# Kernel tuning notes

Measured on AMD Instinct MI355X. Metric: run time of the kernel, lower is better.

Reference implementation:

```python
import jax, jax.numpy as jnp
import numpy as np

D = 128; H = 4; HD = 32; K = 4; OUT = 2; COND = 6; FF = 256

def _ln(x, g, b):
    m = x.mean(-1, keepdims=True)
    v = ((x - m) ** 2).mean(-1, keepdims=True)
    return g * (x - m) * jax.lax.rsqrt(v + 1e-5) + b

def setup_inputs() -> dict:
    key = jax.random.key(0)
    ks = jax.random.split(key, 40)
    B, S = 4096, 128
    def w(k, shape, scale=0.05):
        return (jax.random.normal(k, shape, dtype=jnp.float32) * scale)
    inp = {
        'x': jax.random.normal(ks[0], (B, OUT, S), dtype=jnp.float32),
        'timesteps': jax.random.randint(ks[1], (B,), 0, 1000, dtype=jnp.int32),
        'conditions': jax.random.normal(ks[2], (B, S, COND), dtype=jnp.float32),
        # time embedding MLP: Linear(128->256), SiLU, Linear(256->128)
        't_w1': w(ks[3], (D, 2 * D)), 't_b1': jnp.zeros((2 * D,), jnp.float32),
        't_w2': w(ks[4], (2 * D, D)), 't_b2': jnp.zeros((D,), jnp.float32),
        # condition MLP: Linear(6->64), SiLU, Linear(64->128), SiLU
        'c_w1': w(ks[5], (COND, D // 2)), 'c_b1': jnp.zeros((D // 2,), jnp.float32),
        'c_w2': w(ks[6], (D // 2, D)), 'c_b2': jnp.zeros((D,), jnp.float32),
        # 2 transformer encoder layers (post-norm, relu FFN, dropout=0 eval)
        'attn_wqkv': w(ks[7], (2, D, 3 * D)), 'attn_bqkv': jnp.zeros((2, 3 * D), jnp.float32),
        'attn_wo': w(ks[8], (2, D, D)), 'attn_bo': jnp.zeros((2, D), jnp.float32),
        'ln1_g': jnp.ones((2, D), jnp.float32), 'ln1_b': jnp.zeros((2, D), jnp.float32),
        'ff_w1': w(ks[9], (2, D, FF)), 'ff_b1': jnp.zeros((2, FF), jnp.float32),
        'ff_w2': w(ks[10], (2, FF, D)), 'ff_b2': jnp.zeros((2, D), jnp.float32),
        'ln2_g': jnp.ones((2, D), jnp.float32), 'ln2_b': jnp.zeros((2, D), jnp.float32),
        # mixture weights net: Linear(256->128), SiLU, Linear(128->4), Softmax
        'mw_w1': w(ks[11], (2 * D, D)), 'mw_b1': jnp.zeros((D,), jnp.float32),
        'mw_w2': w(ks[12], (D, K)), 'mw_b2': jnp.zeros((K,), jnp.float32),
        # K student networks: Linear(2+256->128), Tanh, Linear(128->2)
        's_w1': w(ks[13], (K, OUT + 2 * D, D)), 's_b1': jnp.zeros((K, D), jnp.float32),
        's_w2': w(ks[14], (K, D, OUT)), 's_b2': jnp.zeros((K, OUT), jnp.float32),
    }
    return inp

def reference(x, timesteps, conditions, t_w1, t_b1, t_w2, t_b2, c_w1, c_b1, c_w2, c_b2,
              attn_wqkv, attn_bqkv, attn_wo, attn_bo, ln1_g, ln1_b, ff_w1, ff_b1,
              ff_w2, ff_b2, ln2_g, ln2_b, mw_w1, mw_b1, mw_w2, mw_b2,
              s_w1, s_b1, s_w2, s_b2):
    B, _, S = x.shape
    # sinusoidal time embedding
    half = D // 2
    freqs = jnp.exp(-jnp.log(jnp.float32(10000.0)) * jnp.arange(half, dtype=jnp.float32) / half)
    args = timesteps.astype(jnp.float32)[:, None] * freqs[None, :]
    te = jnp.concatenate([jnp.cos(args), jnp.sin(args)], axis=-1)            # [B, D]
    time_emb = jax.nn.silu(te @ t_w1 + t_b1) @ t_w2 + t_b2                   # [B, D]
    # condition embedding MLP
    h = jax.nn.silu(conditions @ c_w1 + c_b1)
    h = jax.nn.silu(h @ c_w2 + c_b2)                                          # [B, S, D]
    # 2-layer transformer encoder (post-norm)
    for l in range(2):
        qkv = h @ attn_wqkv[l] + attn_bqkv[l]                                 # [B, S, 3D]
        q, k, v = jnp.split(qkv, 3, axis=-1)
        q = q.reshape(B, S, H, HD); k = k.reshape(B, S, H, HD); v = v.reshape(B, S, H, HD)
        sc = jnp.einsum('bqhd,bkhd->bhqk', q, k) / jnp.sqrt(jnp.float32(HD))
        a = jax.nn.softmax(sc, axis=-1)
        o = jnp.einsum('bhqk,bkhd->bqhd', a, v).reshape(B, S, D)
        o = o @ attn_wo[l] + attn_bo[l]
        h = _ln(h + o, ln1_g[l], ln1_b[l])
        f = jax.nn.relu(h @ ff_w1[l] + ff_b1[l]) @ ff_w2[l] + ff_b2[l]
        h = _ln(h + f, ln2_g[l], ln2_b[l])
    cond_emb = h.mean(axis=1)                                                 # [B, D]
    combined = jnp.concatenate([time_emb, cond_emb], axis=-1)                 # [B, 2D]
    mw = jax.nn.softmax(jax.nn.silu(combined @ mw_w1 + mw_b1) @ mw_w2 + mw_b2, axis=-1)  # [B, K]
    # students over all seq positions (vectorized over original seq loop)
    xt = jnp.transpose(x, (0, 2, 1))                                          # [B, S, OUT]
    emb_bs = jnp.broadcast_to(combined[:, None, :], (B, S, 2 * D))
    inp = jnp.concatenate([xt, emb_bs], axis=-1)                              # [B, S, OUT+2D]
    hk = jnp.tanh(jnp.einsum('bsi,kio->bsko', inp, s_w1) + s_b1)              # [B, S, K, D]
    ok = jnp.einsum('bsko,koj->bskj', hk, s_w2) + s_b2                        # [B, S, K, OUT]
    out = jnp.einsum('bskj,bk->bsj', ok, mw)                                  # [B, S, OUT]
    return jnp.transpose(out, (0, 2, 1))                                      # [B, OUT, S]
```

## Files before the change

kernel.cpp:

```cpp
#include <hip/hip_runtime.h>

typedef _Float16 hf;
typedef _Float16 hf4 __attribute__((ext_vector_type(4)));
typedef _Float16 hf8 __attribute__((ext_vector_type(8)));
typedef float f4 __attribute__((ext_vector_type(4)));

#define NTH 512
#define ACT_OFF 0
#define P_OFF   32768
#define SC_OFF  40960
#define SMEM_BYTES 73728

#define WSH_QKV 0
#define WSH_WO  98304
#define WSH_FW1 131072
#define WSH_FW2 196608
#define WSH_CW2 262144
#define WSH_TOTAL 270336
#define CEMB_BYTE_OFF 540672

__device__ __forceinline__ float dsilu(float x){ return x / (1.f + __expf(-x)); }
__device__ __forceinline__ float dtanh(float x){
  float xc = fminf(fmaxf(x, -10.f), 10.f);
  float e = __expf(2.f * xc);
  return (e - 1.f) / (e + 1.f);
}

__global__ void prep_pack(const float* __restrict__ wqkv, const float* __restrict__ wo,
                          const float* __restrict__ fw1, const float* __restrict__ fw2,
                          const float* __restrict__ cw2, hf* __restrict__ ws){
  int idx = blockIdx.x * 256 + threadIdx.x;
  if (idx >= WSH_TOTAL) return;
  float v;
  if (idx < WSH_WO){
    int u = idx; int lh = u / 12288; int l = lh >> 2, h = lh & 3;
    int r = u % 12288; int tl = r >> 9; int lane = (r >> 3) & 63; int j = r & 7;
    int q = lane >> 4, c = lane & 15;
    int tn = tl >> 2, tk = tl & 3;
    int k = tk*32 + q*8 + j, nloc = tn*16 + c;
    int gcol = (nloc >> 5)*128 + h*32 + (nloc & 31);
    v = wqkv[l*49152 + k*384 + gcol];
  } else if (idx < WSH_FW1){
    int u = idx - WSH_WO; int l = u >> 14; int r = u & 16383;
    int tl = r >> 9; int lane = (r >> 3) & 63; int j = r & 7;
    int q = lane >> 4, c = lane & 15;
    int tn = tl >> 2, tk = tl & 3;
    v = wo[l*16384 + (tk*32 + q*8 + j)*128 + tn*16 + c];
  } else if (idx < WSH_FW2){
    int u = idx - WSH_FW1; int lch = u >> 14; int l = lch >> 1, ch = lch & 1; int r = u & 16383;
    int tl = r >> 9; int lane = (r >> 3) & 63; int j = r & 7;
    int q = lane >> 4, c = lane & 15;
    int tn = tl >> 2, tk = tl & 3;
    v = fw1[l*32768 + (tk*32 + q*8 + j)*256 + ch*128 + tn*16 + c];
  } else if (idx < WSH_CW2){
    int u = idx - WSH_FW2; int lch = u >> 14; int l = lch >> 1, ch = lch & 1; int r = u & 16383;
    int tl = r >> 9; int lane = (r >> 3) & 63; int j = r & 7;
    int q = lane >> 4, c = lane & 15;
    int tn = tl >> 2, tk = tl & 3;
    v = fw2[l*32768 + (ch*128 + tk*32 + q*8 + j)*128 + tn*16 + c];
  } else {
    int u = idx - WSH_CW2;
    int tl = u >> 9; int lane = (u >> 3) & 63; int j = u & 7;
    int q = lane >> 4, c = lane & 15;
    int tn = tl >> 1, tk = tl & 1;
    v = cw2[(tk*32 + q*8 + j)*128 + tn*16 + c];
  }
  ws[idx] = (hf)v;
}

template<int KT>
__device__ __forceinline__ void gemmN(f4 (&acc)[8], const hf* __restrict__ Ag, const hf* Bh,
                                      int nt, int lane){
#pragma unroll
  for (int tk = 0; tk < KT; ++tk){
    hf8 a = *(const hf8*)(Ag + ((nt*KT + tk) << 9) + lane*8);
#pragma unroll
    for (int ts = 0; ts < 8; ++ts){
      hf8 b = *(const hf8*)(Bh + ((ts*KT + tk) << 9) + lane*8);
      acc[ts] = __builtin_amdgcn_mfma_f32_16x16x32_f16(a, b, acc[ts], 0, 0, 0);
    }
  }
}

__device__ __forceinline__ void store_packed_b64(hf* dst, int KtilesOut, int ts, int ft,
                                                 f4 v, int q, int c){
  int tk = ft >> 1;
  int qp = ((ft & 1) << 1) + (q >> 1);
  int j0 = (q & 1) << 2;
  hf4 h; h[0] = (hf)v[0]; h[1] = (hf)v[1]; h[2] = (hf)v[2]; h[3] = (hf)v[3];
  *(hf4*)(dst + ((ts*KtilesOut + tk) << 9) + ((qp*16 + c) << 3) + j0) = h;
}

__device__ __forceinline__ void ln_pass(hf* A, const hf* Dh, const float* __restrict__ g,
                                        const float* __restrict__ bb, int t){
  int s = t >> 2, p = t & 3;
  float xr[4][8];
  int offs[4];
  float sum = 0.f, sq = 0.f;
#pragma unroll
  for (int tk = 0; tk < 4; ++tk){
    int off = (((s >> 4) * 4 + tk) << 9) + ((p * 16 + (s & 15)) << 3);
    offs[tk] = off;
    hf8 va = *(const hf8*)(A + off);
    hf8 vd = *(const hf8*)(Dh + off);
#pragma unroll
    for (int j = 0; j < 8; ++j){
      float x = (float)va[j] + (float)vd[j];
      xr[tk][j] = x; sum += x; sq += x * x;
    }
  }
  sum += __shfl_xor(sum, 1); sq += __shfl_xor(sq, 1);
  sum += __shfl_xor(sum, 2); sq += __shfl_xor(sq, 2);
  float mean = sum * (1.f/128.f);
  float rstd = rsqrtf(sq * (1.f/128.f) - mean*mean + 1e-5f);
#pragma unroll
  for (int tk = 0; tk < 4; ++tk){
    int f0 = tk*32 + p*8;
    f4 g0 = *(const f4*)(g + f0); f4 g1 = *(const f4*)(g + f0 + 4);
    f4 b0 = *(const f4*)(bb + f0); f4 b1 = *(const f4*)(bb + f0 + 4);
    hf8 y;
#pragma unroll
    for (int j = 0; j < 4; ++j){
      y[j]     = (hf)((xr[tk][j]     - mean) * rstd * g0[j] + b0[j]);
      y[j + 4] = (hf)((xr[tk][j + 4] - mean) * rstd * g1[j] + b1[j]);
    }
    *(hf8*)(A + offs[tk]) = y;
  }
}

__global__ __launch_bounds__(NTH, 4) void fused_fp(
    const float* __restrict__ cond,
    const float* __restrict__ c_w1, const float* __restrict__ c_b1, const float* __restrict__ c_b2,
    const float* __restrict__ bqkv_g, const float* __restrict__ bo_g,
    const float* __restrict__ ln1g_g, const float* __restrict__ ln1b_g,
    const float* __restrict__ fb1_g, const float* __restrict__ fb2_g,
    const float* __restrict__ ln2g_g, const float* __restrict__ ln2b_g,
    const hf* __restrict__ wsp, float* __restrict__ cemb)
{
  extern __shared__ char smem[];
  hf* ACTh = (hf*)(smem + ACT_OFF);
  hf* Ph   = (hf*)(smem + P_OFF);
  hf* SCh  = (hf*)(smem + SC_OFF);
  float* SCf = (float*)(smem + SC_OFF);
  hf* Qh  = SCh;
  hf* Kh  = (hf*)(smem + SC_OFF + 8192);
  hf* VTh = (hf*)(smem + SC_OFF + 16384);
  float* cst  = SCf + 4096;
  float* cw1s = SCf + 4096 + 768;

  const int b = blockIdx.x;
  const int t = threadIdx.x;
  const int w = t >> 6, lane = t & 63, q = lane >> 4, c = lane & 15;
  const int sp = w & 3, np = w >> 2;

  for (int idx = t; idx < 768; idx += NTH) cst[idx] = cond[b * 768 + idx];
  if (t < 384) cw1s[t] = c_w1[t];
  if (t < 64)  cw1s[384 + t] = c_b1[t];
  __syncthreads();

  for (int idx = t; idx < 8192; idx += NTH){
    int s = idx >> 6, jf = idx & 63;
    float a = cw1s[384 + jf];
#pragma unroll
    for (int cc = 0; cc < 6; ++cc) a += cst[s * 6 + cc] * cw1s[cc * 64 + jf];
    SCh[(((s >> 4)*2 + (jf >> 5)) << 9) + ((((jf & 31) >> 3)*16 + (s & 15)) << 3) + (jf & 7)] = (hf)dsilu(a);
  }
  __syncthreads();

  {
    f4 acc[8];
#pragma unroll
    for (int i = 0; i < 8; ++i){ f4 z = {0.f,0.f,0.f,0.f}; acc[i] = z; }
    gemmN<2>(acc, wsp + WSH_CW2, SCh, w, lane);
    f4 cb = *(const f4*)(c_b2 + w*16 + q*4);
#pragma unroll
    for (int ts = 0; ts < 8; ++ts){
      f4 v = acc[ts];
#pragma unroll
      for (int r = 0; r < 4; ++r) v[r] = dsilu(v[r] + cb[r]);
      store_packed_b64(ACTh, 4, ts, w, v, q, c);
    }
  }

  for (int l = 0; l < 2; ++l){
    f4 oacc[8];
#pragma unroll
    for (int i = 0; i < 8; ++i){ f4 z = {0.f,0.f,0.f,0.f}; oacc[i] = z; }

    for (int h = 0; h < 4; ++h){
      __syncthreads();
      {
        const hf* Aq = wsp + WSH_QKV + (l*4 + h)*12288;
        f4 acc[2][3];
#pragma unroll
        for (int i = 0; i < 2; ++i)
#pragma unroll
          for (int j = 0; j < 3; ++j){ f4 z = {0.f,0.f,0.f,0.f}; acc[i][j] = z; }
#pragma unroll
        for (int tk = 0; tk < 4; ++tk){
          hf8 b0 = *(const hf8*)(ACTh + (((2*sp  )*4 + tk) << 9) + lane*8);
          hf8 b1 = *(const hf8*)(ACTh + (((2*sp+1)*4 + tk) << 9) + lane*8);
#pragma unroll
          for (int jn = 0; jn < 3; ++jn){
            hf8 a = *(const hf8*)(Aq + (((np*3 + jn)*4 + tk) << 9) + lane*8);
            acc[0][jn] = __builtin_amdgcn_mfma_f32_16x16x32_f16(a, b0, acc[0][jn], 0, 0, 0);
            acc[1][jn] = __builtin_amdgcn_mfma_f32_16x16x32_f16(a, b1, acc[1][jn], 0, 0, 0);
          }
        }
#pragma unroll
        for (int si = 0; si < 2; ++si)
#pragma unroll
          for (int jn = 0; jn < 3; ++jn){
            int ft = np*3 + jn, ts = 2*sp + si;
            int sel = ft >> 1;
            f4 v = acc[si][jn];
            f4 bq = *(const f4*)(bqkv_g + l*384 + sel*128 + h*32 + (ft & 1)*16 + q*4);
#pragma unroll
            for (int r = 0; r < 4; ++r) v[r] += bq[r];
            if (sel == 0){
#pragma unroll
              for (int r = 0; r < 4; ++r) v[r] *= 0.17677669529663687f;
              store_packed_b64(Qh, 1, ts, ft, v, q, c);
            } else if (sel == 1){
              store_packed_b64(Kh, 1, ts, ft - 2, v, q, c);
            } else {
              int td = ft - 4;
              int qp = ((ts & 1) << 1) + (c >> 3);
              hf* pb = VTh + ((td*4 + (ts >> 1)) << 9) + (c & 7);
#pragma unroll
              for (int r = 0; r < 4; ++r) pb[(qp*16 + q*4 + r) << 3] = (hf)v[r];
            }
          }
      }
      __syncthreads();
      {
        hf8 qf = *(const hf8*)(Qh + (w << 9) + lane*8);
        f4 sc[8];
#pragma unroll
        for (int kst = 0; kst < 8; ++kst){
          hf8 kv = *(const hf8*)(Kh + (kst << 9) + lane*8);
          f4 z = {0.f,0.f,0.f,0.f};
          sc[kst] = __builtin_amdgcn_mfma_f32_16x16x32_f16(kv, qf, z, 0, 0, 0);
        }
        float m = -1e30f;
#pragma unroll
        for (int kst = 0; kst < 8; ++kst)
#pragma unroll
          for (int r = 0; r < 4; ++r) m = fmaxf(m, sc[kst][r]);
        m = fmaxf(m, __shfl_xor(m, 16));
        m = fmaxf(m, __shfl_xor(m, 32));
        float ls = 0.f;
#pragma unroll
        for (int kst = 0; kst < 8; ++kst)
#pragma unroll
          for (int r = 0; r < 4; ++r){
            float e = __expf(sc[kst][r] - m);
            sc[kst][r] = e; ls += e;
          }
        ls += __shfl_xor(ls, 16);
        ls += __shfl_xor(ls, 32);
        float rl = 1.f / ls;
        hf* Pw = Ph + (w << 9);
#pragma unroll
        for (int ks = 0; ks < 4; ++ks){
#pragma unroll
          for (int h2 = 0; h2 < 2; ++h2){
            int kst = 2*ks + h2;
            int qp = h2*2 + (q >> 1);
            int j0 = (q & 1) << 2;
            hf4 pv;
#pragma unroll
            for (int r = 0; r < 4; ++r) pv[r] = (hf)(sc[kst][r] * rl);
            *(hf4*)(Pw + qp*128 + c*8 + j0) = pv;
          }
          hf8 bp = *(const hf8*)(Pw + lane*8);
          hf8 a0 = *(const hf8*)(VTh + ((     ks) << 9) + lane*8);
          hf8 a1 = *(const hf8*)(VTh + ((4 +  ks) << 9) + lane*8);
          oacc[2*h]     = __builtin_amdgcn_mfma_f32_16x16x32_f16(a0, bp, oacc[2*h],     0, 0, 0);
          oacc[2*h + 1] = __builtin_amdgcn_mfma_f32_16x16x32_f16(a1, bp, oacc[2*h + 1], 0, 0, 0);
        }
      }
    }

    __syncthreads();
#pragma unroll
    for (int ft = 0; ft < 8; ++ft) store_packed_b64(SCh, 4, w, ft, oacc[ft], q, c);
    __syncthreads();

    {
      f4 acc[8];
#pragma unroll
      for (int i = 0; i < 8; ++i){ f4 z = {0.f,0.f,0.f,0.f}; acc[i] = z; }
      gemmN<4>(acc, wsp + WSH_WO + l*16384, SCh, w, lane);
      __syncthreads();
      f4 bo = *(const f4*)(bo_g + l*128 + w*16 + q*4);
#pragma unroll
      for (int ts = 0; ts < 8; ++ts){
        f4 v = acc[ts];
#pragma unroll
        for (int r = 0; r < 4; ++r) v[r] += bo[r];
        store_packed_b64(SCh, 4, ts, w, v, q, c);
      }
    }
    __syncthreads();
    ln_pass(ACTh, SCh, ln1g_g + l*128, ln1b_g + l*128, t);
    __syncthreads();

    {
      f4 facc[8];
#pragma unroll
      for (int i = 0; i < 8; ++i){ f4 z = {0.f,0.f,0.f,0.f}; facc[i] = z; }
      for (int ch = 0; ch < 2; ++ch){
        f4 acc[8];
#pragma unroll
        for (int i = 0; i < 8; ++i){ f4 z = {0.f,0.f,0.f,0.f}; acc[i] = z; }
        gemmN<4>(acc, wsp + WSH_FW1 + (l*2 + ch)*16384, ACTh, w, lane);
        f4 fb = *(const f4*)(fb1_g + l*256 + ch*128 + w*16 + q*4);
#pragma unroll
        for (int ts = 0; ts < 8; ++ts){
          f4 v = acc[ts];
#pragma unroll
          for (int r = 0; r < 4; ++r) v[r] = fmaxf(v[r] + fb[r], 0.f);
          store_packed_b64(SCh, 4, ts, w, v, q, c);
        }
        __syncthreads();
        gemmN<4>(facc, wsp + WSH_FW2 + (l*2 + ch)*16384, SCh, w, lane);
        __syncthreads();
      }
      f4 fb2 = *(const f4*)(fb2_g + l*128 + w*16 + q*4);
#pragma unroll
      for (int ts = 0; ts < 8; ++ts){
        f4 v = facc[ts];
#pragma unroll
        for (int r = 0; r < 4; ++r) v[r] += fb2[r];
        store_packed_b64(SCh, 4, ts, w, v, q, c);
      }
    }
    __syncthreads();
    ln_pass(ACTh, SCh, ln2g_g + l*128, ln2b_g + l*128, t);
    __syncthreads();
  }

  {
    int o = t & 15;
    float fs[8];
#pragma unroll
    for (int j = 0; j < 8; ++j) fs[j] = 0.f;
#pragma unroll
    for (int u = 0; u < 4; ++u){
      int s = (t >> 4)*4 + u;
      hf8 v = *(const hf8*)(ACTh + (((s >> 4)*4 + (o >> 2)) << 9) + (((o & 3)*16 + (s & 15)) << 3));
#pragma unroll
      for (int j = 0; j < 8; ++j) fs[j] += (float)v[j];
    }
#pragma unroll
    for (int j = 0; j < 8; ++j){
      fs[j] += __shfl_xor(fs[j], 16);
      fs[j] += __shfl_xor(fs[j], 32);
    }
    if (lane < 16){
      f4 v0, v1;
#pragma unroll
      for (int j = 0; j < 4; ++j){ v0[j] = fs[j]; v1[j] = fs[j+4]; }
      *(f4*)(SCf + w*128 + o*8)     = v0;
      *(f4*)(SCf + w*128 + o*8 + 4) = v1;
    }
  }
  __syncthreads();
  if (t < 128){
    float a = 0.f;
#pragma unroll
    for (int wv = 0; wv < 8; ++wv) a += SCf[wv*128 + t];
    cemb[b*128 + t] = a * (1.f/128.f);
  }
}

__global__ __launch_bounds__(256, 4) void tail_k(
    const float* __restrict__ x, const int* __restrict__ tstep, const float* __restrict__ cemb,
    const float* __restrict__ t_w1, const float* __restrict__ t_b1,
    const float* __restrict__ t_w2, const float* __restrict__ t_b2,
    const float* __restrict__ mw_w1, const float* __restrict__ mw_b1,
    const float* __restrict__ mw_w2, const float* __restrict__ mw_b2,
    const float* __restrict__ s_w1, const float* __restrict__ s_b1,
    const float* __restrict__ s_w2, const float* __restrict__ s_b2,
    float* __restrict__ out)
{
  __shared__ float sw01[1024], sw2[1024];
  __shared__ float te[128], th[256], comb[256], mwh[128], mwls[8], cvec[512], okp[1024];
  const int t = threadIdx.x;

  for (int i = t; i < 1024; i += 256){
    int row = i >> 9, k = (i >> 7) & 3, j = i & 127;
    sw01[i] = s_w1[k*33024 + row*128 + j];
    sw2[i]  = s_w2[i];
  }
  __syncthreads();

  for (int bi = 0; bi < 8; ++bi){
    int b = blockIdx.x * 8 + bi;
    if (t < 128){
      int i = t & 63;
      float f = __expf(-logf(10000.f) * (float)i * (1.f/64.f));
      float a = (float)tstep[b] * f;
      te[t] = (t < 64) ? cosf(a) : sinf(a);
    }
    __syncthreads();
    {
      float a = t_b1[t];
      for (int i = 0; i < 128; ++i) a += te[i] * t_w1[i*256 + t];
      th[t] = dsilu(a);
    }
    __syncthreads();
    if (t < 128){
      float a = t_b2[t];
      for (int j = 0; j < 256; ++j) a += th[j] * t_w2[j*128 + t];
      comb[t] = a;
    } else {
      comb[t] = cemb[b*128 + t - 128];
    }
    __syncthreads();
    if (t < 128){
      float a = mw_b1[t];
      for (int i = 0; i < 256; ++i) a += comb[i] * mw_w1[i*128 + t];
      mwh[t] = dsilu(a);
    }
#pragma unroll
    for (int u = 0; u < 2; ++u){
      int o = t + u*256; int k = o >> 7, j = o & 127;
      float a = s_b1[k*128 + j];
      for (int i = 0; i < 256; ++i) a += comb[i] * s_w1[k*33024 + (2 + i)*128 + j];
      cvec[o] = a;
    }
    __syncthreads();
    if (t < 4){
      float a = mw_b2[t];
      for (int j = 0; j < 128; ++j) a += mwh[j] * mw_w2[j*4 + t];
      mwls[4 + t] = a;
    }
    __syncthreads();
    if (t == 0){
      float mx = fmaxf(fmaxf(mwls[4], mwls[5]), fmaxf(mwls[6], mwls[7]));
      float e0 = __expf(mwls[4] - mx), e1 = __expf(mwls[5] - mx);
      float e2 = __expf(mwls[6] - mx), e3 = __expf(mwls[7] - mx);
      float rs = 1.f / (e0 + e1 + e2 + e3);
      mwls[0] = e0*rs; mwls[1] = e1*rs; mwls[2] = e2*rs; mwls[3] = e3*rs;
    }
#pragma unroll
    for (int u = 0; u < 2; ++u){
      int o = t + u*256; int k = o >> 7, s = o & 127;
      float x0 = x[b*256 + s];
      float x1 = x[b*256 + 128 + s];
      float a0 = 0.f, a1 = 0.f;
      for (int j = 0; j < 128; ++j){
        float hk = dtanh(cvec[k*128 + j] + x0*sw01[k*128 + j] + x1*sw01[512 + k*128 + j]);
        a0 += hk * sw2[k*256 + 2*j];
        a1 += hk * sw2[k*256 + 2*j + 1];
      }
      okp[k*256 + s]       = a0 + s_b2[2*k];
      okp[k*256 + 128 + s] = a1 + s_b2[2*k + 1];
    }
    __syncthreads();
    {
      int row = t >> 7, s = t & 127;
      float a = 0.f;
#pragma unroll
      for (int k = 0; k < 4; ++k) a += mwls[k] * okp[k*256 + row*128 + s];
      out[b*256 + row*128 + s] = a;
    }
    __syncthreads();
  }
}

extern "C" void kernel_launch(void* const* d_in, const int* in_sizes, int n_in,
                              void* d_out, int out_size, void* d_ws, size_t ws_size,
                              hipStream_t stream){
  (void)n_in; (void)ws_size; (void)out_size;
  hipFuncSetAttribute((const void*)fused_fp, hipFuncAttributeMaxDynamicSharedMemorySize, SMEM_BYTES);
  int B = in_sizes[1];
  hf* wsp = (hf*)d_ws;
  float* cemb = (float*)((char*)d_ws + CEMB_BYTE_OFF);
  prep_pack<<<dim3((WSH_TOTAL + 255) / 256), dim3(256), 0, stream>>>(
      (const float*)d_in[11], (const float*)d_in[13], (const float*)d_in[17],
      (const float*)d_in[19], (const float*)d_in[9], wsp);
  fused_fp<<<dim3(B), dim3(NTH), SMEM_BYTES, stream>>>(
      (const float*)d_in[2],
      (const float*)d_in[7], (const float*)d_in[8], (const float*)d_in[10],
      (const float*)d_in[12], (const float*)d_in[14],
      (const float*)d_in[15], (const float*)d_in[16],
      (const float*)d_in[18], (const float*)d_in[20],
      (const float*)d_in[21], (const float*)d_in[22],
      wsp, cemb);
  tail_k<<<dim3(B / 8), dim3(256), 0, stream>>>(
      (const float*)d_in[0], (const int*)d_in[1], cemb,
      (const float*)d_in[3], (const float*)d_in[4], (const float*)d_in[5], (const float*)d_in[6],
      (const float*)d_in[23], (const float*)d_in[24], (const float*)d_in[25], (const float*)d_in[26],
      (const float*)d_in[27], (const float*)d_in[28], (const float*)d_in[29], (const float*)d_in[30],
      (float*)d_out);
}
```

Before: 1.201 ms.

## Fuse time-embedding, mixture and student tail into the per-sample transformer kernel

```diff
diff --git a/kernel.cpp b/kernel.cpp
--- a/kernel.cpp
+++ b/kernel.cpp
@@ -9,7 +9,8 @@
 #define ACT_OFF 0
 #define P_OFF   32768
 #define SC_OFF  40960
-#define SMEM_BYTES 73728
+#define COMB_OFF 73728
+#define SMEM_BYTES 74752
 
 #define WSH_QKV 0
 #define WSH_WO  98304
@@ -17,7 +18,6 @@
 #define WSH_FW2 196608
 #define WSH_CW2 262144
 #define WSH_TOTAL 270336
-#define CEMB_BYTE_OFF 540672
 
 __device__ __forceinline__ float dsilu(float x){ return x / (1.f + __expf(-x)); }
 __device__ __forceinline__ float dtanh(float x){
@@ -129,24 +129,39 @@
 }
 
 __global__ __launch_bounds__(NTH, 4) void fused_fp(
-    const float* __restrict__ cond,
+    const float* __restrict__ x, const int* __restrict__ tstep, const float* __restrict__ cond,
+    const float* __restrict__ t_w1, const float* __restrict__ t_b1,
+    const float* __restrict__ t_w2, const float* __restrict__ t_b2,
     const float* __restrict__ c_w1, const float* __restrict__ c_b1, const float* __restrict__ c_b2,
     const float* __restrict__ bqkv_g, const float* __restrict__ bo_g,
     const float* __restrict__ ln1g_g, const float* __restrict__ ln1b_g,
     const float* __restrict__ fb1_g, const float* __restrict__ fb2_g,
     const float* __restrict__ ln2g_g, const float* __restrict__ ln2b_g,
-    const hf* __restrict__ wsp, float* __restrict__ cemb)
+    const float* __restrict__ mw_w1, const float* __restrict__ mw_b1,
+    const float* __restrict__ mw_w2, const float* __restrict__ mw_b2,
+    const float* __restrict__ s_w1, const float* __restrict__ s_b1,
+    const float* __restrict__ s_w2, const float* __restrict__ s_b2,
+    const hf* __restrict__ wsp, float* __restrict__ out)
 {
   extern __shared__ char smem[];
   hf* ACTh = (hf*)(smem + ACT_OFF);
   hf* Ph   = (hf*)(smem + P_OFF);
   hf* SCh  = (hf*)(smem + SC_OFF);
   float* SCf = (float*)(smem + SC_OFF);
+  float* comb = (float*)(smem + COMB_OFF);
   hf* Qh  = SCh;
   hf* Kh  = (hf*)(smem + SC_OFF + 8192);
   hf* VTh = (hf*)(smem + SC_OFF + 16384);
   float* cst  = SCf + 4096;
-  float* cw1s = SCf + 4096 + 768;
+  float* cw1s = SCf + 4864;
+  float* te   = SCf + 5312;
+  float* th   = SCf + 5440;
+  float* sw01 = SCf;
+  float* sw2t = SCf + 1024;
+  float* cvec = SCf + 2048;
+  float* okp  = SCf + 2560;
+  float* mwh  = SCf + 3584;
+  float* mwls = SCf + 3712;
 
   const int b = blockIdx.x;
   const int t = threadIdx.x;
@@ -156,6 +171,12 @@
   for (int idx = t; idx < 768; idx += NTH) cst[idx] = cond[b * 768 + idx];
   if (t < 384) cw1s[t] = c_w1[t];
   if (t < 64)  cw1s[384 + t] = c_b1[t];
+  if (t < 128){
+    int i = t & 63;
+    float f = __expf(-logf(10000.f) * (float)i * (1.f/64.f));
+    float a = (float)tstep[b] * f;
+    te[t] = (t < 64) ? cosf(a) : sinf(a);
+  }
   __syncthreads();
 
   for (int idx = t; idx < 8192; idx += NTH){
@@ -165,6 +186,11 @@
     for (int cc = 0; cc < 6; ++cc) a += cst[s * 6 + cc] * cw1s[cc * 64 + jf];
     SCh[(((s >> 4)*2 + (jf >> 5)) << 9) + ((((jf & 31) >> 3)*16 + (s & 15)) << 3) + (jf & 7)] = (hf)dsilu(a);
   }
+  if (t < 256){
+    float a = t_b1[t];
+    for (int i = 0; i < 128; ++i) a += te[i] * t_w1[i*256 + t];
+    th[t] = dsilu(a);
+  }
   __syncthreads();
 
   {
@@ -180,6 +206,11 @@
       for (int r = 0; r < 4; ++r) v[r] = dsilu(v[r] + cb[r]);
       store_packed_b64(ACTh, 4, ts, w, v, q, c);
     }
+  }
+  if (t < 128){
+    float a = t_b2[t];
+    for (int j = 0; j < 256; ++j) a += th[j] * t_w2[j*128 + t];
+    comb[t] = a;
   }
 
   for (int l = 0; l < 2; ++l){
@@ -371,103 +402,57 @@
     float a = 0.f;
 #pragma unroll
     for (int wv = 0; wv < 8; ++wv) a += SCf[wv*128 + t];
-    cemb[b*128 + t] = a * (1.f/128.f);
-  }
-}
-
-__global__ __launch_bounds__(256, 4) void tail_k(
-    const float* __restrict__ x, const int* __restrict__ tstep, const float* __restrict__ cemb,
-    const float* __restrict__ t_w1, const float* __restrict__ t_b1,
-    const float* __restrict__ t_w2, const float* __restrict__ t_b2,
-    const float* __restrict__ mw_w1, const float* __restrict__ mw_b1,
-    const float* __restrict__ mw_w2, const float* __restrict__ mw_b2,
-    const float* __restrict__ s_w1, const float* __restrict__ s_b1,
-    const float* __restrict__ s_w2, const float* __restrict__ s_b2,
-    float* __restrict__ out)
-{
-  __shared__ float sw01[1024], sw2[1024];
-  __shared__ float te[128], th[256], comb[256], mwh[128], mwls[8], cvec[512], okp[1024];
-  const int t = threadIdx.x;
-
-  for (int i = t; i < 1024; i += 256){
+    comb[128 + t] = a * (1.f/128.f);
+  }
+  __syncthreads();
+
+  for (int i = t; i < 1024; i += NTH){
     int row = i >> 9, k = (i >> 7) & 3, j = i & 127;
     sw01[i] = s_w1[k*33024 + row*128 + j];
-    sw2[i]  = s_w2[i];
-  }
-  __syncthreads();
-
-  for (int bi = 0; bi < 8; ++bi){
-    int b = blockIdx.x * 8 + bi;
-    if (t < 128){
-      int i = t & 63;
-      float f = __expf(-logf(10000.f) * (float)i * (1.f/64.f));
-      float a = (float)tstep[b] * f;
-      te[t] = (t < 64) ? cosf(a) : sinf(a);
-    }
-    __syncthreads();
-    {
-      float a = t_b1[t];
-      for (int i = 0; i < 128; ++i) a += te[i] * t_w1[i*256 + t];
-      th[t] = dsilu(a);
-    }
-    __syncthreads();
-    if (t < 128){
-      float a = t_b2[t];
-      for (int j = 0; j < 256; ++j) a += th[j] * t_w2[j*128 + t];
-      comb[t] = a;
-    } else {
-      comb[t] = cemb[b*128 + t - 128];
-    }
-    __syncthreads();
-    if (t < 128){
-      float a = mw_b1[t];
-      for (int i = 0; i < 256; ++i) a += comb[i] * mw_w1[i*128 + t];
-      mwh[t] = dsilu(a);
-    }
-#pragma unroll
-    for (int u = 0; u < 2; ++u){
-      int o = t + u*256; int k = o >> 7, j = o & 127;
-      float a = s_b1[k*128 + j];
-      for (int i = 0; i < 256; ++i) a += comb[i] * s_w1[k*33024 + (2 + i)*128 + j];
-      cvec[o] = a;
-    }
-    __syncthreads();
-    if (t < 4){
-      float a = mw_b2[t];
-      for (int j = 0; j < 128; ++j) a += mwh[j] * mw_w2[j*4 + t];
-      mwls[4 + t] = a;
-    }
-    __syncthreads();
-    if (t == 0){
-      float mx = fmaxf(fmaxf(mwls[4], mwls[5]), fmaxf(mwls[6], mwls[7]));
-      float e0 = __expf(mwls[4] - mx), e1 = __expf(mwls[5] - mx);
-      float e2 = __expf(mwls[6] - mx), e3 = __expf(mwls[7] - mx);
-      float rs = 1.f / (e0 + e1 + e2 + e3);
-      mwls[0] = e0*rs; mwls[1] = e1*rs; mwls[2] = e2*rs; mwls[3] = e3*rs;
-    }
-#pragma unroll
-    for (int u = 0; u < 2; ++u){
-      int o = t + u*256; int k = o >> 7, s = o & 127;
-      float x0 = x[b*256 + s];
-      float x1 = x[b*256 + 128 + s];
-      float a0 = 0.f, a1 = 0.f;
-      for (int j = 0; j < 128; ++j){
-        float hk = dtanh(cvec[k*128 + j] + x0*sw01[k*128 + j] + x1*sw01[512 + k*128 + j]);
-        a0 += hk * sw2[k*256 + 2*j];
-        a1 += hk * sw2[k*256 + 2*j + 1];
-      }
-      okp[k*256 + s]       = a0 + s_b2[2*k];
-      okp[k*256 + 128 + s] = a1 + s_b2[2*k + 1];
-    }
-    __syncthreads();
-    {
-      int row = t >> 7, s = t & 127;
-      float a = 0.f;
-#pragma unroll
-      for (int k = 0; k < 4; ++k) a += mwls[k] * okp[k*256 + row*128 + s];
-      out[b*256 + row*128 + s] = a;
-    }
-    __syncthreads();
+    sw2t[i] = s_w2[i];
+  }
+  if (t < 128){
+    float a = mw_b1[t];
+    for (int i = 0; i < 256; ++i) a += comb[i] * mw_w1[i*128 + t];
+    mwh[t] = dsilu(a);
+  }
+  {
+    int k = t >> 7, j = t & 127;
+    float a = s_b1[k*128 + j];
+    for (int i = 0; i < 256; ++i) a += comb[i] * s_w1[k*33024 + (2 + i)*128 + j];
+    cvec[t] = a;
+  }
+  __syncthreads();
+
+  if (t < 4){
+    float a = mw_b2[t];
+    for (int j = 0; j < 128; ++j) a += mwh[j] * mw_w2[j*4 + t];
+    mwls[t] = a;
+  }
+  {
+    int k = t >> 7, s = t & 127;
+    float x0 = x[b*256 + s];
+    float x1 = x[b*256 + 128 + s];
+    float a0 = 0.f, a1 = 0.f;
+    for (int j = 0; j < 128; ++j){
+      float hk = dtanh(cvec[k*128 + j] + x0*sw01[k*128 + j] + x1*sw01[512 + k*128 + j]);
+      a0 += hk * sw2t[k*256 + 2*j];
+      a1 += hk * sw2t[k*256 + 2*j + 1];
+    }
+    okp[k*256 + s]       = a0 + s_b2[2*k];
+    okp[k*256 + 128 + s] = a1 + s_b2[2*k + 1];
+  }
+  __syncthreads();
+
+  if (t < 256){
+    int row = t >> 7, s = t & 127;
+    float l0 = mwls[0], l1 = mwls[1], l2 = mwls[2], l3 = mwls[3];
+    float mx = fmaxf(fmaxf(l0, l1), fmaxf(l2, l3));
+    float e0 = __expf(l0 - mx), e1 = __expf(l1 - mx), e2 = __expf(l2 - mx), e3 = __expf(l3 - mx);
+    float rs = 1.f / (e0 + e1 + e2 + e3);
+    float a = e0*okp[0*256 + row*128 + s] + e1*okp[1*256 + row*128 + s]
+            + e2*okp[2*256 + row*128 + s] + e3*okp[3*256 + row*128 + s];
+    out[b*256 + row*128 + s] = a * rs;
   }
 }
 
@@ -478,22 +463,18 @@
   hipFuncSetAttribute((const void*)fused_fp, hipFuncAttributeMaxDynamicSharedMemorySize, SMEM_BYTES);
   int B = in_sizes[1];
   hf* wsp = (hf*)d_ws;
-  float* cemb = (float*)((char*)d_ws + CEMB_BYTE_OFF);
   prep_pack<<<dim3((WSH_TOTAL + 255) / 256), dim3(256), 0, stream>>>(
       (const float*)d_in[11], (const float*)d_in[13], (const float*)d_in[17],
       (const float*)d_in[19], (const float*)d_in[9], wsp);
   fused_fp<<<dim3(B), dim3(NTH), SMEM_BYTES, stream>>>(
-      (const float*)d_in[2],
+      (const float*)d_in[0], (const int*)d_in[1], (const float*)d_in[2],
+      (const float*)d_in[3], (const float*)d_in[4], (const float*)d_in[5], (const float*)d_in[6],
       (const float*)d_in[7], (const float*)d_in[8], (const float*)d_in[10],
       (const float*)d_in[12], (const float*)d_in[14],
       (const float*)d_in[15], (const float*)d_in[16],
       (const float*)d_in[18], (const float*)d_in[20],
       (const float*)d_in[21], (const float*)d_in[22],
-      wsp, cemb);
-  tail_k<<<dim3(B / 8), dim3(256), 0, stream>>>(
-      (const float*)d_in[0], (const int*)d_in[1], cemb,
-      (const float*)d_in[3], (const float*)d_in[4], (const float*)d_in[5], (const float*)d_in[6],
       (const float*)d_in[23], (const float*)d_in[24], (const float*)d_in[25], (const float*)d_in[26],
       (const float*)d_in[27], (const float*)d_in[28], (const float*)d_in[29], (const float*)d_in[30],
-      (float*)d_out);
-}
+      wsp, (float*)d_out);
+}
```

Result: no change. 1.209 ms (+0.6%).

## Launch one tail block per batch row and shorten its serial sync chain

Applied to the files above, without the earlier changes.

```diff
diff --git a/kernel.cpp b/kernel.cpp
--- a/kernel.cpp
+++ b/kernel.cpp
@@ -146,7 +146,7 @@
   hf* Kh  = (hf*)(smem + SC_OFF + 8192);
   hf* VTh = (hf*)(smem + SC_OFF + 16384);
   float* cst  = SCf + 4096;
-  float* cw1s = SCf + 4096 + 768;
+  float* cw1s = SCf + 4864;
 
   const int b = blockIdx.x;
   const int t = threadIdx.x;
@@ -375,7 +375,7 @@
   }
 }
 
-__global__ __launch_bounds__(256, 4) void tail_k(
+__global__ __launch_bounds__(256, 8) void tail_k(
     const float* __restrict__ x, const int* __restrict__ tstep, const float* __restrict__ cemb,
     const float* __restrict__ t_w1, const float* __restrict__ t_b1,
     const float* __restrict__ t_w2, const float* __restrict__ t_b2,
@@ -385,8 +385,9 @@
     const float* __restrict__ s_w2, const float* __restrict__ s_b2,
     float* __restrict__ out)
 {
-  __shared__ float sw01[1024], sw2[1024];
-  __shared__ float te[128], th[256], comb[256], mwh[128], mwls[8], cvec[512], okp[1024];
+  __shared__ float te[128], th[256], comb[256], sw01[1024], sw2[1024];
+  __shared__ float cvec[512], okp[1024], mwh[128], mwls[4];
+  const int b = blockIdx.x;
   const int t = threadIdx.x;
 
   for (int i = t; i < 1024; i += 256){
@@ -394,80 +395,88 @@
     sw01[i] = s_w1[k*33024 + row*128 + j];
     sw2[i]  = s_w2[i];
   }
-  __syncthreads();
-
-  for (int bi = 0; bi < 8; ++bi){
-    int b = blockIdx.x * 8 + bi;
-    if (t < 128){
-      int i = t & 63;
-      float f = __expf(-logf(10000.f) * (float)i * (1.f/64.f));
-      float a = (float)tstep[b] * f;
-      te[t] = (t < 64) ? cosf(a) : sinf(a);
-    }
-    __syncthreads();
-    {
-      float a = t_b1[t];
-      for (int i = 0; i < 128; ++i) a += te[i] * t_w1[i*256 + t];
-      th[t] = dsilu(a);
-    }
-    __syncthreads();
-    if (t < 128){
-      float a = t_b2[t];
-      for (int j = 0; j < 256; ++j) a += th[j] * t_w2[j*128 + t];
-      comb[t] = a;
-    } else {
-      comb[t] = cemb[b*128 + t - 128];
-    }
-    __syncthreads();
-    if (t < 128){
-      float a = mw_b1[t];
-      for (int i = 0; i < 256; ++i) a += comb[i] * mw_w1[i*128 + t];
-      mwh[t] = dsilu(a);
-    }
-#pragma unroll
-    for (int u = 0; u < 2; ++u){
-      int o = t + u*256; int k = o >> 7, j = o & 127;
-      float a = s_b1[k*128 + j];
-      for (int i = 0; i < 256; ++i) a += comb[i] * s_w1[k*33024 + (2 + i)*128 + j];
-      cvec[o] = a;
-    }
-    __syncthreads();
-    if (t < 4){
-      float a = mw_b2[t];
-      for (int j = 0; j < 128; ++j) a += mwh[j] * mw_w2[j*4 + t];
-      mwls[4 + t] = a;
-    }
-    __syncthreads();
-    if (t == 0){
-      float mx = fmaxf(fmaxf(mwls[4], mwls[5]), fmaxf(mwls[6], mwls[7]));
-      float e0 = __expf(mwls[4] - mx), e1 = __expf(mwls[5] - mx);
-      float e2 = __expf(mwls[6] - mx), e3 = __expf(mwls[7] - mx);
-      float rs = 1.f / (e0 + e1 + e2 + e3);
-      mwls[0] = e0*rs; mwls[1] = e1*rs; mwls[2] = e2*rs; mwls[3] = e3*rs;
-    }
-#pragma unroll
-    for (int u = 0; u < 2; ++u){
-      int o = t + u*256; int k = o >> 7, s = o & 127;
-      float x0 = x[b*256 + s];
-      float x1 = x[b*256 + 128 + s];
-      float a0 = 0.f, a1 = 0.f;
-      for (int j = 0; j < 128; ++j){
-        float hk = dtanh(cvec[k*128 + j] + x0*sw01[k*128 + j] + x1*sw01[512 + k*128 + j]);
-        a0 += hk * sw2[k*256 + 2*j];
-        a1 += hk * sw2[k*256 + 2*j + 1];
-      }
-      okp[k*256 + s]       = a0 + s_b2[2*k];
-      okp[k*256 + 128 + s] = a1 + s_b2[2*k + 1];
-    }
-    __syncthreads();
-    {
-      int row = t >> 7, s = t & 127;
-      float a = 0.f;
-#pragma unroll
-      for (int k = 0; k < 4; ++k) a += mwls[k] * okp[k*256 + row*128 + s];
-      out[b*256 + row*128 + s] = a;
-    }
-    __syncthreads();
+  if (t < 128){
+    int i = t & 63;
+    float f = __expf(-logf(10000.f) * (float)i * (1.f/64.f));
+    float a = (float)tstep[b] * f;
+    te[t] = (t < 64) ? cosf(a) : sinf(a);
+    comb[128 + t] = cemb[b*128 + t];
+  }
+  __syncthreads();
+
+  {
+    float a = t_b1[t];
+    for (int i = 0; i < 128; ++i) a += te[i] * t_w1[i*256 + t];
+    th[t] = dsilu(a);
+  }
+  __syncthreads();
+  if (t < 128){
+    float a = t_b2[t];
+    for (int i = 0; i < 256; ++i) a += th[i] * t_w2[i*128 + t];
+    comb[t] = a;
+  }
+  __syncthreads();
+
+  {
+    int k = t >> 7, j = t & 127;
+    float a0 = s_b1[k*128 + j], a1 = s_b1[(k + 2)*128 + j];
+    const float* w0 = s_w1 + k*33024 + 256 + j;
+    const float* w1 = s_w1 + (k + 2)*33024 + 256 + j;
+    for (int i = 0; i < 256; ++i){
+      float cb = comb[i];
+      a0 += cb * w0[i*128];
+      a1 += cb * w1[i*128];
+    }
+    cvec[k*128 + j] = a0;
+    cvec[(k + 2)*128 + j] = a1;
+  }
+  if (t < 128){
+    float a = mw_b1[t];
+    for (int i = 0; i < 256; ++i) a += comb[i] * mw_w1[i*128 + t];
+    mwh[t] = dsilu(a);
+  }
+  __syncthreads();
+
+  if (t < 64){
+    int cc = t & 3, j0 = t >> 2;
+    float a = 0.f;
+#pragma unroll
+    for (int i = 0; i < 8; ++i){
+      int j = j0 + 16*i;
+      a += mwh[j] * mw_w2[j*4 + cc];
+    }
+    a += __shfl_xor(a, 4);
+    a += __shfl_xor(a, 8);
+    a += __shfl_xor(a, 16);
+    a += __shfl_xor(a, 32);
+    if (t < 4) mwls[t] = a + mw_b2[t];
+  }
+
+#pragma unroll
+  for (int u = 0; u < 2; ++u){
+    int o = t + u*256, k = o >> 7, s = o & 127;
+    float x0 = x[b*256 + s];
+    float x1 = x[b*256 + 128 + s];
+    float a0 = 0.f, a1 = 0.f;
+    for (int j = 0; j < 128; ++j){
+      float hk = dtanh(cvec[k*128 + j] + x0*sw01[k*128 + j] + x1*sw01[512 + k*128 + j]);
+      a0 += hk * sw2[k*256 + 2*j];
+      a1 += hk * sw2[k*256 + 2*j + 1];
+    }
+    okp[k*256 + s]       = a0 + s_b2[2*k];
+    okp[k*256 + 128 + s] = a1 + s_b2[2*k + 1];
+  }
+  __syncthreads();
+
+  {
+    int row = t >> 7, s = t & 127;
+    float l0 = mwls[0], l1 = mwls[1], l2 = mwls[2], l3 = mwls[3];
+    float mx = fmaxf(fmaxf(l0, l1), fmaxf(l2, l3));
+    float e0 = __expf(l0 - mx), e1 = __expf(l1 - mx), e2 = __expf(l2 - mx), e3 = __expf(l3 - mx);
+    float rs = 1.f / (e0 + e1 + e2 + e3);
+    float a = e0*okp[0*256 + row*128 + s] + e1*okp[1*256 + row*128 + s]
+            + e2*okp[2*256 + row*128 + s] + e3*okp[3*256 + row*128 + s];
+    out[b*256 + row*128 + s] = a * rs;
   }
 }
 
@@ -490,7 +499,7 @@
       (const float*)d_in[18], (const float*)d_in[20],
       (const float*)d_in[21], (const float*)d_in[22],
       wsp, cemb);
-  tail_k<<<dim3(B / 8), dim3(256), 0, stream>>>(
+  tail_k<<<dim3(B), dim3(256), 0, stream>>>(
       (const float*)d_in[0], (const int*)d_in[1], cemb,
       (const float*)d_in[3], (const float*)d_in[4], (const float*)d_in[5], (const float*)d_in[6],
       (const float*)d_in[23], (const float*)d_in[24], (const float*)d_in[25], (const float*)d_in[26],
```

Result: faster. 1.125 ms (-6.4%).
